# Kernel tuning notes

Measured on AMD Instinct MI355X. Metric: run time of the kernel, lower is better.

The kernel has to match this reference:

```python
import jax, jax.numpy as jnp
import numpy as np

N_BATCH = 128   # C: number of PWL channels / generator batch
N_PTS = 32768   # N: samples per channel
K_PWL = 20      # breakpoints per piecewise-linear function
LATENT = 8
HID = 8
EPS = 1e-7


def _mlp(z, W1, b1, W2, b2):
    # torch mlp: Linear -> Tanh -> Linear -> Tanh
    h = jnp.tanh(z @ W1 + b1)
    return jnp.tanh(h @ W2 + b2)


def _normalize01(a):
    # per-row min/max normalization, a: [C, N]
    a = a - a.min(axis=1, keepdims=True)
    return a / a.max(axis=1, keepdims=True)


def _calibrate1d(x, xp, yp):
    # x: [N, C], xp/yp: [C, K]
    N, C = x.shape
    K = xp.shape[1]
    bp = jnp.concatenate([x[:, :, None], jnp.broadcast_to(xp[None], (N, C, K))], axis=2)  # [N,C,K+1]
    order = jnp.argsort(bp, axis=2)                       # [N,C,K+1]
    sorted_bp = jnp.take_along_axis(bp, order, axis=2)
    x_idx = jnp.argmin(order, axis=2)                     # rank of x among breakpoints
    cand = x_idx - 1
    start_idx = jnp.where(x_idx == 0, 1, jnp.where(x_idx == K, K - 2, cand))
    end_idx = jnp.where(start_idx == cand, start_idx + 2, start_idx + 1)
    start_x = jnp.take_along_axis(sorted_bp, start_idx[..., None], axis=2)[..., 0]
    end_x = jnp.take_along_axis(sorted_bp, end_idx[..., None], axis=2)[..., 0]
    start_idx2 = jnp.where(x_idx == 0, 0, jnp.where(x_idx == K, K - 2, cand))
    yp_e = jnp.broadcast_to(yp[None], (N, C, K))
    start_y = jnp.take_along_axis(yp_e, start_idx2[..., None], axis=2)[..., 0]
    end_y = jnp.take_along_axis(yp_e, (start_idx2 + 1)[..., None], axis=2)[..., 0]
    return start_y + (x - start_x) * (end_y - start_y) / (end_x - start_x + EPS)


def setup_inputs() -> dict:
    key = jax.random.key(0)
    ks = jax.random.split(key, 16)
    s = 0.5
    f32 = jnp.float32
    return {
        "zf": jax.random.normal(ks[0], (N_BATCH, LATENT), f32),
        "zx": jax.random.normal(ks[1], (N_BATCH, N_PTS, LATENT), f32),
        "ze": jax.random.normal(ks[2], (N_BATCH, N_PTS, LATENT), f32),
        "Wx1": jax.random.normal(ks[3], (LATENT, HID), f32) * s,
        "bx1": jax.random.normal(ks[4], (HID,), f32) * s,
        "Wx2": jax.random.normal(ks[5], (HID, 1), f32) * s,
        "bx2": jax.random.normal(ks[6], (1,), f32) * s,
        "We1": jax.random.normal(ks[7], (LATENT, HID), f32) * s,
        "be1": jax.random.normal(ks[8], (HID,), f32) * s,
        "We2": jax.random.normal(ks[9], (HID, 1), f32) * s,
        "be2": jax.random.normal(ks[10], (1,), f32) * s,
        "Wf1": jax.random.normal(ks[11], (LATENT, HID), f32) * s,
        "bf1": jax.random.normal(ks[12], (HID,), f32) * s,
        "Wf2": jax.random.normal(ks[13], (HID, K_PWL), f32) * s,
        "bf2": jax.random.normal(ks[14], (K_PWL,), f32) * s,
        "directions": jax.random.randint(ks[15], (N_BATCH,), 0, 2) > 0,
    }


def reference(zf, zx, ze, Wx1, bx1, Wx2, bx2, We1, be1, We2, be2, Wf1, bf1, Wf2, bf2, directions):
    # gen_f: random ascending/descending monotone PWL per channel
    pts = _mlp(zf, Wf1, bf1, Wf2, bf2)                        # [C, K]
    asc = jnp.sort(pts, axis=1)
    yp = jnp.where(directions[:, None], asc, asc[:, ::-1])    # [C, K]
    xp = jnp.broadcast_to(jnp.linspace(0.0, 1.0, K_PWL, dtype=pts.dtype)[None, :], yp.shape)
    # forward_x: cause variable, per-channel normalized to [0,1]
    x = _mlp(zx, Wx1, bx1, Wx2, bx2)[..., 0]                  # [C, N]
    x = _normalize01(x).T                                     # [N, C]
    # forward_e: standardized noise (global mean / unbiased std)
    e = _mlp(ze, We1, be1, We2, be2)[..., 0].T                # [N, C]
    e = (e - e.mean()) / e.std(ddof=1)
    # forward_y
    y = _calibrate1d(x, xp, yp) + 0.1 * e                     # [N, C]
    return y
```

## Files before the change

kernel.cpp:

```cpp
#include <hip/hip_runtime.h>

#define C_CH  128
#define NP    32768
#define K_PWL 20
#define LAT   8
#define HID   8
#define SLOTS 32

__device__ __forceinline__ float fast_tanh(float x) {
    float e = __expf(2.0f * x);
    return fmaf(-2.0f, __builtin_amdgcn_rcpf(e + 1.0f), 1.0f);
}

__device__ __forceinline__ unsigned fenc(float f) {
    unsigned u = __float_as_uint(f);
    return (u & 0x80000000u) ? ~u : (u | 0x80000000u);
}
__device__ __forceinline__ float fdec(unsigned e) {
    unsigned u = (e & 0x80000000u) ? (e ^ 0x80000000u) : ~e;
    return __uint_as_float(u);
}

__global__ void prep(const float* __restrict__ zf,
                     const float* __restrict__ Wf1, const float* __restrict__ bf1,
                     const float* __restrict__ Wf2, const float* __restrict__ bf2,
                     const unsigned char* __restrict__ dirs_raw,
                     float* __restrict__ ypw,
                     unsigned* cminE, unsigned* cmaxE, double* sums) {
    int t = threadIdx.x;
    if (t < C_CH) { cminE[t] = 0xFFFFFFFFu; cmaxE[t] = 0u; }
    if (t < 2 * SLOTS) sums[t] = 0.0;

    __shared__ int is_i32;
    if (t == 0) {
        const int* di = (const int*)dirs_raw;
        int ok = 1;
        for (int i = 0; i < 32; i++) { int v = di[i]; if (v != 0 && v != 1) ok = 0; }
        is_i32 = ok;
    }
    __syncthreads();
    if (t >= C_CH) return;
    int c = t;

    float z[LAT];
    #pragma unroll
    for (int l = 0; l < LAT; l++) z[l] = zf[c * LAT + l];
    float h[HID];
    #pragma unroll
    for (int j = 0; j < HID; j++) {
        float a = bf1[j];
        #pragma unroll
        for (int l = 0; l < LAT; l++) a = fmaf(z[l], Wf1[l * HID + j], a);
        h[j] = fast_tanh(a);
    }
    float p[K_PWL];
    #pragma unroll
    for (int k = 0; k < K_PWL; k++) {
        float a = bf2[k];
        #pragma unroll
        for (int j = 0; j < HID; j++) a = fmaf(h[j], Wf2[j * K_PWL + k], a);
        p[k] = fast_tanh(a);
    }
    for (int i = 1; i < K_PWL; i++) {
        float key = p[i];
        int j = i - 1;
        while (j >= 0 && p[j] > key) { p[j + 1] = p[j]; j--; }
        p[j + 1] = key;
    }
    int dir = is_i32 ? (((const int*)dirs_raw)[c] != 0) : (dirs_raw[c] != 0);
    for (int k = 0; k < K_PWL; k++)
        ypw[c * K_PWL + k] = dir ? p[k] : p[K_PWL - 1 - k];
}

__global__ __launch_bounds__(256, 8)
void pass1(const float* __restrict__ zx, const float* __restrict__ ze,
           const float* __restrict__ Wx1, const float* __restrict__ bx1,
           const float* __restrict__ Wx2, const float* __restrict__ bx2,
           const float* __restrict__ We1, const float* __restrict__ be1,
           const float* __restrict__ We2, const float* __restrict__ be2,
           float2* __restrict__ xe,
           unsigned* __restrict__ cminE, unsigned* __restrict__ cmaxE,
           double* __restrict__ sums) {
    __shared__ float szx[LAT][256];
    __shared__ float sze[LAT][256];
    __shared__ float sw[162];

    int t = threadIdx.x;
    if (t < 64)       sw[t] = Wx1[t];
    else if (t < 72)  sw[t] = bx1[t - 64];
    else if (t < 80)  sw[t] = Wx2[t - 72];
    else if (t == 80) sw[80] = bx2[0];
    else if (t < 145) sw[t] = We1[t - 81];
    else if (t < 153) sw[t] = be1[t - 145];
    else if (t < 161) sw[t] = We2[t - 153];
    else if (t == 161) sw[161] = be2[0];

    int c = blockIdx.y;
    size_t row = (size_t)c * NP;
    int tile0 = blockIdx.x * 256;
    const float4* zx4 = (const float4*)(zx + (row + tile0) * LAT);
    const float4* ze4 = (const float4*)(ze + (row + tile0) * LAT);

    float4 vx0 = zx4[t];
    float4 vx1 = zx4[256 + t];
    float4 ve0 = ze4[t];
    float4 ve1 = ze4[256 + t];

    {
        int q = t, p = q >> 1, l0 = (q & 1) * 4;
        szx[l0 + 0][p] = vx0.x; szx[l0 + 1][p] = vx0.y;
        szx[l0 + 2][p] = vx0.z; szx[l0 + 3][p] = vx0.w;
        sze[l0 + 0][p] = ve0.x; sze[l0 + 1][p] = ve0.y;
        sze[l0 + 2][p] = ve0.z; sze[l0 + 3][p] = ve0.w;
    }
    {
        int q = 256 + t, p = q >> 1, l0 = (q & 1) * 4;
        szx[l0 + 0][p] = vx1.x; szx[l0 + 1][p] = vx1.y;
        szx[l0 + 2][p] = vx1.z; szx[l0 + 3][p] = vx1.w;
        sze[l0 + 0][p] = ve1.x; sze[l0 + 1][p] = ve1.y;
        sze[l0 + 2][p] = ve1.z; sze[l0 + 3][p] = ve1.w;
    }
    __syncthreads();

    float ix[LAT], ie[LAT];
    #pragma unroll
    for (int l = 0; l < LAT; l++) { ix[l] = szx[l][t]; ie[l] = sze[l][t]; }

    float xacc = sw[80];
    float eacc = sw[161];
    #pragma unroll
    for (int j = 0; j < HID; j++) {
        float hx = sw[64 + j];
        float he = sw[145 + j];
        #pragma unroll
        for (int l = 0; l < LAT; l++) {
            hx = fmaf(ix[l], sw[l * 8 + j], hx);
            he = fmaf(ie[l], sw[81 + l * 8 + j], he);
        }
        xacc = fmaf(fast_tanh(hx), sw[72 + j], xacc);
        eacc = fmaf(fast_tanh(he), sw[153 + j], eacc);
    }
    float xv = fast_tanh(xacc);
    float ev = fast_tanh(eacc);

    xe[row + tile0 + t] = make_float2(xv, ev);

    float mn = xv, mx = xv, s = ev, s2 = ev * ev;
    #pragma unroll
    for (int o = 32; o > 0; o >>= 1) {
        mn = fminf(mn, __shfl_down(mn, o));
        mx = fmaxf(mx, __shfl_down(mx, o));
        s += __shfl_down(s, o);
        s2 += __shfl_down(s2, o);
    }
    __shared__ float rmn[4], rmx[4], rs[4], rs2[4];
    int wave = t >> 6, lane = t & 63;
    if (lane == 0) { rmn[wave] = mn; rmx[wave] = mx; rs[wave] = s; rs2[wave] = s2; }
    __syncthreads();
    if (t == 0) {
        for (int w = 1; w < 4; w++) {
            mn = fminf(mn, rmn[w]); mx = fmaxf(mx, rmx[w]);
            s += rs[w]; s2 += rs2[w];
        }
        atomicMin(&cminE[c], fenc(mn));
        atomicMax(&cmaxE[c], fenc(mx));
        int slot = (blockIdx.x + blockIdx.y) & (SLOTS - 1);
        atomicAdd(&sums[2 * slot], (double)s);
        atomicAdd(&sums[2 * slot + 1], (double)s2);
    }
}

__global__ __launch_bounds__(256)
void pass2(const float2* __restrict__ xe, const float* __restrict__ ypw,
           const unsigned* __restrict__ cminE, const unsigned* __restrict__ cmaxE,
           const double* __restrict__ sums,
           float* __restrict__ out) {
    __shared__ float ytile[C_CH * 33];
    __shared__ float syp[C_CH * K_PWL];
    __shared__ float smin[C_CH], sinv[C_CH];
    __shared__ float sstat[2];

    int t = threadIdx.x;
    for (int i = t; i < C_CH * K_PWL; i += 256) syp[i] = ypw[i];
    if (t < C_CH) {
        float mn = fdec(cminE[t]);
        float mx = fdec(cmaxE[t]);
        smin[t] = mn;
        sinv[t] = __builtin_amdgcn_rcpf(mx - mn);
    }
    if (t == 0) {
        double s = 0.0, s2 = 0.0;
        for (int i = 0; i < SLOTS; i++) { s += sums[2 * i]; s2 += sums[2 * i + 1]; }
        double M = (double)C_CH * NP;
        double mean = s / M;
        double var = (s2 - s * s / M) / (M - 1.0);
        sstat[0] = (float)mean;
        sstat[1] = (float)(0.1 / sqrt(var));
    }
    __syncthreads();

    const float INV_DENOM = 1.0f / (1.0f / 19.0f + 1e-7f);
    float mean = sstat[0], escale = sstat[1];
    int n0 = blockIdx.x * 32;

    #pragma unroll
    for (int i = 0; i < 16; i++) {
        int idx = i * 256 + t;
        int c = idx >> 5;
        int j = idx & 31;
        float2 v = xe[(size_t)c * NP + (n0 + j)];
        float xn = (v.x - smin[c]) * sinv[c];
        int seg = (int)floorf(xn * 19.0f);
        seg = max(0, min(18, seg));
        float y0 = syp[c * K_PWL + seg];
        float y1 = syp[c * K_PWL + seg + 1];
        float y = fmaf((xn - (float)seg * (1.0f / 19.0f)) * INV_DENOM, y1 - y0, y0);
        y = fmaf(v.y - mean, escale, y);
        ytile[c * 33 + j] = y;
    }
    __syncthreads();
    #pragma unroll
    for (int i = 0; i < 16; i++) {
        int idx = i * 256 + t;
        int j = idx >> 7;
        int c = idx & 127;
        out[(size_t)(n0 + j) * C_CH + c] = ytile[c * 33 + j];
    }
}

extern "C" void kernel_launch(void* const* d_in, const int* in_sizes, int n_in,
                              void* d_out, int out_size, void* d_ws, size_t ws_size,
                              hipStream_t stream) {
    const float* zf  = (const float*)d_in[0];
    const float* zx  = (const float*)d_in[1];
    const float* ze  = (const float*)d_in[2];
    const float* Wx1 = (const float*)d_in[3];
    const float* bx1 = (const float*)d_in[4];
    const float* Wx2 = (const float*)d_in[5];
    const float* bx2 = (const float*)d_in[6];
    const float* We1 = (const float*)d_in[7];
    const float* be1 = (const float*)d_in[8];
    const float* We2 = (const float*)d_in[9];
    const float* be2 = (const float*)d_in[10];
    const float* Wf1 = (const float*)d_in[11];
    const float* bf1 = (const float*)d_in[12];
    const float* Wf2 = (const float*)d_in[13];
    const float* bf2 = (const float*)d_in[14];
    const unsigned char* dirs = (const unsigned char*)d_in[15];

    float2* xe  = (float2*)d_ws;
    float*  ypw = (float*)(xe + (size_t)C_CH * NP);
    unsigned* cminE = (unsigned*)(ypw + C_CH * K_PWL);
    unsigned* cmaxE = cminE + C_CH;
    double* sums = (double*)(cmaxE + C_CH);

    hipLaunchKernelGGL(prep, dim3(1), dim3(256), 0, stream,
                       zf, Wf1, bf1, Wf2, bf2, dirs, ypw, cminE, cmaxE, sums);
    hipLaunchKernelGGL(pass1, dim3(NP / 256, C_CH), dim3(256), 0, stream,
                       zx, ze, Wx1, bx1, Wx2, bx2, We1, be1, We2, be2,
                       xe, cminE, cmaxE, sums);
    hipLaunchKernelGGL(pass2, dim3(NP / 32), dim3(256), 0, stream,
                       xe, ypw, cminE, cmaxE, sums, (float*)d_out);
}
```

Measured before the change: 366.8 us.

## Make pass1 persistent-style with register prefetch and two points per thread

Pass1 now has each block loop over 8 tiles of 512 points, with each thread computing two points per iteration straight from registers. The LDS transpose of the latent inputs is removed. The next iteration's float4 loads are software-prefetched into registers while the current MLP runs, and the weights are laid out so they can be read as float4 from LDS. The grid is 8x smaller, so there are fewer per-block atomics and reductions. In exchange, register pressure is higher (launch bounds relaxed to 4 blocks) and fewer blocks are available to hide latency.

```diff
diff --git a/kernel.cpp b/kernel.cpp
--- a/kernel.cpp
+++ b/kernel.cpp
@@ -6,6 +6,7 @@
 #define LAT   8
 #define HID   8
 #define SLOTS 32
+#define T_ITER 8
 
 __device__ __forceinline__ float fast_tanh(float x) {
     float e = __expf(2.0f * x);
@@ -72,7 +73,7 @@
         ypw[c * K_PWL + k] = dir ? p[k] : p[K_PWL - 1 - k];
 }
 
-__global__ __launch_bounds__(256, 8)
+__global__ __launch_bounds__(256, 4)
 void pass1(const float* __restrict__ zx, const float* __restrict__ ze,
            const float* __restrict__ Wx1, const float* __restrict__ bx1,
            const float* __restrict__ Wx2, const float* __restrict__ bx2,
@@ -81,71 +82,96 @@
            float2* __restrict__ xe,
            unsigned* __restrict__ cminE, unsigned* __restrict__ cmaxE,
            double* __restrict__ sums) {
-    __shared__ float szx[LAT][256];
-    __shared__ float sze[LAT][256];
-    __shared__ float sw[162];
+    __shared__ __align__(16) float swx1[HID][LAT];
+    __shared__ __align__(16) float swe1[HID][LAT];
+    __shared__ float sbx1[HID], swx2[HID], sbe1[HID], swe2[HID];
+    __shared__ float sb2[2];
 
     int t = threadIdx.x;
-    if (t < 64)       sw[t] = Wx1[t];
-    else if (t < 72)  sw[t] = bx1[t - 64];
-    else if (t < 80)  sw[t] = Wx2[t - 72];
-    else if (t == 80) sw[80] = bx2[0];
-    else if (t < 145) sw[t] = We1[t - 81];
-    else if (t < 153) sw[t] = be1[t - 145];
-    else if (t < 161) sw[t] = We2[t - 153];
-    else if (t == 161) sw[161] = be2[0];
+    if (t < 64)        { swx1[t & 7][t >> 3] = Wx1[t]; }
+    else if (t < 128)  { int u = t - 64; swe1[u & 7][u >> 3] = We1[u]; }
+    else if (t < 136)  sbx1[t - 128] = bx1[t - 128];
+    else if (t < 144)  swx2[t - 136] = Wx2[t - 136];
+    else if (t < 152)  sbe1[t - 144] = be1[t - 144];
+    else if (t < 160)  swe2[t - 152] = We2[t - 152];
+    else if (t == 160) sb2[0] = bx2[0];
+    else if (t == 161) sb2[1] = be2[0];
+    __syncthreads();
 
     int c = blockIdx.y;
     size_t row = (size_t)c * NP;
-    int tile0 = blockIdx.x * 256;
-    const float4* zx4 = (const float4*)(zx + (row + tile0) * LAT);
-    const float4* ze4 = (const float4*)(ze + (row + tile0) * LAT);
-
-    float4 vx0 = zx4[t];
-    float4 vx1 = zx4[256 + t];
-    float4 ve0 = ze4[t];
-    float4 ve1 = ze4[256 + t];
-
+    int base = blockIdx.x * (T_ITER * 512);
+    const float4* zx4 = (const float4*)(zx + (row + base) * LAT);
+    const float4* ze4 = (const float4*)(ze + (row + base) * LAT);
+
+    float4 nx0a, nx0b, nx1a, nx1b, ne0a, ne0b, ne1a, ne1b;
     {
-        int q = t, p = q >> 1, l0 = (q & 1) * 4;
-        szx[l0 + 0][p] = vx0.x; szx[l0 + 1][p] = vx0.y;
-        szx[l0 + 2][p] = vx0.z; szx[l0 + 3][p] = vx0.w;
-        sze[l0 + 0][p] = ve0.x; sze[l0 + 1][p] = ve0.y;
-        sze[l0 + 2][p] = ve0.z; sze[l0 + 3][p] = ve0.w;
-    }
-    {
-        int q = 256 + t, p = q >> 1, l0 = (q & 1) * 4;
-        szx[l0 + 0][p] = vx1.x; szx[l0 + 1][p] = vx1.y;
-        szx[l0 + 2][p] = vx1.z; szx[l0 + 3][p] = vx1.w;
-        sze[l0 + 0][p] = ve1.x; sze[l0 + 1][p] = ve1.y;
-        sze[l0 + 2][p] = ve1.z; sze[l0 + 3][p] = ve1.w;
-    }
-    __syncthreads();
-
-    float ix[LAT], ie[LAT];
-    #pragma unroll
-    for (int l = 0; l < LAT; l++) { ix[l] = szx[l][t]; ie[l] = sze[l][t]; }
-
-    float xacc = sw[80];
-    float eacc = sw[161];
-    #pragma unroll
-    for (int j = 0; j < HID; j++) {
-        float hx = sw[64 + j];
-        float he = sw[145 + j];
+        int qa = 2 * t, qb = 512 + 2 * t;
+        nx0a = zx4[qa]; nx0b = zx4[qa + 1];
+        nx1a = zx4[qb]; nx1b = zx4[qb + 1];
+        ne0a = ze4[qa]; ne0b = ze4[qa + 1];
+        ne1a = ze4[qb]; ne1b = ze4[qb + 1];
+    }
+
+    float bx2s = sb2[0], be2s = sb2[1];
+    float mn = 1e30f, mx = -1e30f, s = 0.f, s2 = 0.f;
+
+    #pragma unroll 1
+    for (int i = 0; i < T_ITER; i++) {
+        float4 cx0a = nx0a, cx0b = nx0b, cx1a = nx1a, cx1b = nx1b;
+        float4 ce0a = ne0a, ce0b = ne0b, ce1a = ne1a, ce1b = ne1b;
+        if (i + 1 < T_ITER) {
+            int qa = (i + 1) * 1024 + 2 * t;
+            int qb = qa + 512;
+            nx0a = zx4[qa]; nx0b = zx4[qa + 1];
+            nx1a = zx4[qb]; nx1b = zx4[qb + 1];
+            ne0a = ze4[qa]; ne0b = ze4[qa + 1];
+            ne1a = ze4[qb]; ne1b = ze4[qb + 1];
+        }
+
+        float xa0 = bx2s, xa1 = bx2s, ea0 = be2s, ea1 = be2s;
         #pragma unroll
-        for (int l = 0; l < LAT; l++) {
-            hx = fmaf(ix[l], sw[l * 8 + j], hx);
-            he = fmaf(ie[l], sw[81 + l * 8 + j], he);
+        for (int j = 0; j < HID; j++) {
+            float4 wxa = *(const float4*)&swx1[j][0];
+            float4 wxb = *(const float4*)&swx1[j][4];
+            float4 wea = *(const float4*)&swe1[j][0];
+            float4 web = *(const float4*)&swe1[j][4];
+            float hx0 = sbx1[j], hx1 = hx0;
+            float he0 = sbe1[j], he1 = he0;
+            hx0 = fmaf(cx0a.x, wxa.x, hx0); hx0 = fmaf(cx0a.y, wxa.y, hx0);
+            hx0 = fmaf(cx0a.z, wxa.z, hx0); hx0 = fmaf(cx0a.w, wxa.w, hx0);
+            hx0 = fmaf(cx0b.x, wxb.x, hx0); hx0 = fmaf(cx0b.y, wxb.y, hx0);
+            hx0 = fmaf(cx0b.z, wxb.z, hx0); hx0 = fmaf(cx0b.w, wxb.w, hx0);
+            hx1 = fmaf(cx1a.x, wxa.x, hx1); hx1 = fmaf(cx1a.y, wxa.y, hx1);
+            hx1 = fmaf(cx1a.z, wxa.z, hx1); hx1 = fmaf(cx1a.w, wxa.w, hx1);
+            hx1 = fmaf(cx1b.x, wxb.x, hx1); hx1 = fmaf(cx1b.y, wxb.y, hx1);
+            hx1 = fmaf(cx1b.z, wxb.z, hx1); hx1 = fmaf(cx1b.w, wxb.w, hx1);
+            he0 = fmaf(ce0a.x, wea.x, he0); he0 = fmaf(ce0a.y, wea.y, he0);
+            he0 = fmaf(ce0a.z, wea.z, he0); he0 = fmaf(ce0a.w, wea.w, he0);
+            he0 = fmaf(ce0b.x, web.x, he0); he0 = fmaf(ce0b.y, web.y, he0);
+            he0 = fmaf(ce0b.z, web.z, he0); he0 = fmaf(ce0b.w, web.w, he0);
+            he1 = fmaf(ce1a.x, wea.x, he1); he1 = fmaf(ce1a.y, wea.y, he1);
+            he1 = fmaf(ce1a.z, wea.z, he1); he1 = fmaf(ce1a.w, wea.w, he1);
+            he1 = fmaf(ce1b.x, web.x, he1); he1 = fmaf(ce1b.y, web.y, he1);
+            he1 = fmaf(ce1b.z, web.z, he1); he1 = fmaf(ce1b.w, web.w, he1);
+            xa0 = fmaf(fast_tanh(hx0), swx2[j], xa0);
+            xa1 = fmaf(fast_tanh(hx1), swx2[j], xa1);
+            ea0 = fmaf(fast_tanh(he0), swe2[j], ea0);
+            ea1 = fmaf(fast_tanh(he1), swe2[j], ea1);
         }
-        xacc = fmaf(fast_tanh(hx), sw[72 + j], xacc);
-        eacc = fmaf(fast_tanh(he), sw[153 + j], eacc);
-    }
-    float xv = fast_tanh(xacc);
-    float ev = fast_tanh(eacc);
-
-    xe[row + tile0 + t] = make_float2(xv, ev);
-
-    float mn = xv, mx = xv, s = ev, s2 = ev * ev;
+        float xv0 = fast_tanh(xa0), xv1 = fast_tanh(xa1);
+        float ev0 = fast_tanh(ea0), ev1 = fast_tanh(ea1);
+
+        int n = base + i * 512 + t;
+        xe[row + n]       = make_float2(xv0, ev0);
+        xe[row + n + 256] = make_float2(xv1, ev1);
+
+        mn = fminf(mn, fminf(xv0, xv1));
+        mx = fmaxf(mx, fmaxf(xv0, xv1));
+        s  += ev0 + ev1;
+        s2 += fmaf(ev0, ev0, ev1 * ev1);
+    }
+
     #pragma unroll
     for (int o = 32; o > 0; o >>= 1) {
         mn = fminf(mn, __shfl_down(mn, o));
@@ -189,11 +215,11 @@
         sinv[t] = __builtin_amdgcn_rcpf(mx - mn);
     }
     if (t == 0) {
-        double s = 0.0, s2 = 0.0;
-        for (int i = 0; i < SLOTS; i++) { s += sums[2 * i]; s2 += sums[2 * i + 1]; }
+        double sd = 0.0, sd2 = 0.0;
+        for (int i = 0; i < SLOTS; i++) { sd += sums[2 * i]; sd2 += sums[2 * i + 1]; }
         double M = (double)C_CH * NP;
-        double mean = s / M;
-        double var = (s2 - s * s / M) / (M - 1.0);
+        double mean = sd / M;
+        double var = (sd2 - sd * sd / M) / (M - 1.0);
         sstat[0] = (float)mean;
         sstat[1] = (float)(0.1 / sqrt(var));
     }
@@ -256,7 +282,7 @@
 
     hipLaunchKernelGGL(prep, dim3(1), dim3(256), 0, stream,
                        zf, Wf1, bf1, Wf2, bf2, dirs, ypw, cminE, cmaxE, sums);
-    hipLaunchKernelGGL(pass1, dim3(NP / 256, C_CH), dim3(256), 0, stream,
+    hipLaunchKernelGGL(pass1, dim3(NP / (T_ITER * 512), C_CH), dim3(256), 0, stream,
                        zx, ze, Wx1, bx1, Wx2, bx2, We1, be1, We2, be2,
                        xe, cminE, cmaxE, sums);
     hipLaunchKernelGGL(pass2, dim3(NP / 32), dim3(256), 0, stream,
```

After: 581.5 us. 58.5% more time.

## Process multiple points per thread in pass1 with direct float4 loads

Applied to the files above, without the earlier changes.

Pass1 now handles 8 points per thread in a loop instead of one. Each thread reads its two float4 latent rows directly from global memory rather than staging them through a shared-memory transpose. The x and e weights are interleaved as float2 in shared memory so one load feeds both MLPs. Per-thread min/max/sum are accumulated across points before the wave reduction, which cuts the number of blocks and atomics by 8x. Per-thread loads are now strided by 32 bytes (two float4 per point), which may lower coalescing efficiency, and the loop uses unroll 1, which limits memory-level parallelism.

```diff
diff --git a/kernel.cpp b/kernel.cpp
--- a/kernel.cpp
+++ b/kernel.cpp
@@ -6,6 +6,7 @@
 #define LAT   8
 #define HID   8
 #define SLOTS 32
+#define PTS   8
 
 __device__ __forceinline__ float fast_tanh(float x) {
     float e = __expf(2.0f * x);
@@ -81,71 +82,58 @@
            float2* __restrict__ xe,
            unsigned* __restrict__ cminE, unsigned* __restrict__ cmaxE,
            double* __restrict__ sums) {
-    __shared__ float szx[LAT][256];
-    __shared__ float sze[LAT][256];
-    __shared__ float sw[162];
+    __shared__ __align__(16) float2 sw1[HID][LAT];
+    __shared__ float2 sb1[HID], sw2[HID];
+    __shared__ float2 sb2;
 
     int t = threadIdx.x;
-    if (t < 64)       sw[t] = Wx1[t];
-    else if (t < 72)  sw[t] = bx1[t - 64];
-    else if (t < 80)  sw[t] = Wx2[t - 72];
-    else if (t == 80) sw[80] = bx2[0];
-    else if (t < 145) sw[t] = We1[t - 81];
-    else if (t < 153) sw[t] = be1[t - 145];
-    else if (t < 161) sw[t] = We2[t - 153];
-    else if (t == 161) sw[161] = be2[0];
+    if (t < 64)        { int l = t >> 3, j = t & 7; sw1[j][l] = make_float2(Wx1[t], We1[t]); }
+    else if (t < 72)   { int j = t - 64; sb1[j] = make_float2(bx1[j], be1[j]); }
+    else if (t < 80)   { int j = t - 72; sw2[j] = make_float2(Wx2[j], We2[j]); }
+    else if (t == 80)  sb2 = make_float2(bx2[0], be2[0]);
+    __syncthreads();
 
     int c = blockIdx.y;
     size_t row = (size_t)c * NP;
-    int tile0 = blockIdx.x * 256;
-    const float4* zx4 = (const float4*)(zx + (row + tile0) * LAT);
-    const float4* ze4 = (const float4*)(ze + (row + tile0) * LAT);
-
-    float4 vx0 = zx4[t];
-    float4 vx1 = zx4[256 + t];
-    float4 ve0 = ze4[t];
-    float4 ve1 = ze4[256 + t];
-
-    {
-        int q = t, p = q >> 1, l0 = (q & 1) * 4;
-        szx[l0 + 0][p] = vx0.x; szx[l0 + 1][p] = vx0.y;
-        szx[l0 + 2][p] = vx0.z; szx[l0 + 3][p] = vx0.w;
-        sze[l0 + 0][p] = ve0.x; sze[l0 + 1][p] = ve0.y;
-        sze[l0 + 2][p] = ve0.z; sze[l0 + 3][p] = ve0.w;
-    }
-    {
-        int q = 256 + t, p = q >> 1, l0 = (q & 1) * 4;
-        szx[l0 + 0][p] = vx1.x; szx[l0 + 1][p] = vx1.y;
-        szx[l0 + 2][p] = vx1.z; szx[l0 + 3][p] = vx1.w;
-        sze[l0 + 0][p] = ve1.x; sze[l0 + 1][p] = ve1.y;
-        sze[l0 + 2][p] = ve1.z; sze[l0 + 3][p] = ve1.w;
-    }
-    __syncthreads();
-
-    float ix[LAT], ie[LAT];
-    #pragma unroll
-    for (int l = 0; l < LAT; l++) { ix[l] = szx[l][t]; ie[l] = sze[l][t]; }
-
-    float xacc = sw[80];
-    float eacc = sw[161];
-    #pragma unroll
-    for (int j = 0; j < HID; j++) {
-        float hx = sw[64 + j];
-        float he = sw[145 + j];
+    int base = blockIdx.x * (256 * PTS);
+    const float4* zx4 = (const float4*)(zx + (row + base) * LAT);
+    const float4* ze4 = (const float4*)(ze + (row + base) * LAT);
+    float2* xeo = xe + row + base;
+
+    float2 b2v = sb2;
+    float mn = 1e30f, mx = -1e30f, s = 0.f, s2 = 0.f;
+
+    #pragma unroll 1
+    for (int i = 0; i < PTS; i++) {
+        int n = i * 256 + t;
+        float4 xa = zx4[2 * n], xb = zx4[2 * n + 1];
+        float4 ea = ze4[2 * n], eb = ze4[2 * n + 1];
+
+        float2 acc = b2v;
         #pragma unroll
-        for (int l = 0; l < LAT; l++) {
-            hx = fmaf(ix[l], sw[l * 8 + j], hx);
-            he = fmaf(ie[l], sw[81 + l * 8 + j], he);
+        for (int j = 0; j < HID; j++) {
+            float2 h = sb1[j];
+            float2 w;
+            w = sw1[j][0]; h.x = fmaf(xa.x, w.x, h.x); h.y = fmaf(ea.x, w.y, h.y);
+            w = sw1[j][1]; h.x = fmaf(xa.y, w.x, h.x); h.y = fmaf(ea.y, w.y, h.y);
+            w = sw1[j][2]; h.x = fmaf(xa.z, w.x, h.x); h.y = fmaf(ea.z, w.y, h.y);
+            w = sw1[j][3]; h.x = fmaf(xa.w, w.x, h.x); h.y = fmaf(ea.w, w.y, h.y);
+            w = sw1[j][4]; h.x = fmaf(xb.x, w.x, h.x); h.y = fmaf(eb.x, w.y, h.y);
+            w = sw1[j][5]; h.x = fmaf(xb.y, w.x, h.x); h.y = fmaf(eb.y, w.y, h.y);
+            w = sw1[j][6]; h.x = fmaf(xb.z, w.x, h.x); h.y = fmaf(eb.z, w.y, h.y);
+            w = sw1[j][7]; h.x = fmaf(xb.w, w.x, h.x); h.y = fmaf(eb.w, w.y, h.y);
+            float2 w2v = sw2[j];
+            acc.x = fmaf(fast_tanh(h.x), w2v.x, acc.x);
+            acc.y = fmaf(fast_tanh(h.y), w2v.y, acc.y);
         }
-        xacc = fmaf(fast_tanh(hx), sw[72 + j], xacc);
-        eacc = fmaf(fast_tanh(he), sw[153 + j], eacc);
-    }
-    float xv = fast_tanh(xacc);
-    float ev = fast_tanh(eacc);
-
-    xe[row + tile0 + t] = make_float2(xv, ev);
-
-    float mn = xv, mx = xv, s = ev, s2 = ev * ev;
+        float xv = fast_tanh(acc.x);
+        float ev = fast_tanh(acc.y);
+
+        xeo[n] = make_float2(xv, ev);
+        mn = fminf(mn, xv); mx = fmaxf(mx, xv);
+        s += ev; s2 = fmaf(ev, ev, s2);
+    }
+
     #pragma unroll
     for (int o = 32; o > 0; o >>= 1) {
         mn = fminf(mn, __shfl_down(mn, o));
@@ -189,11 +177,11 @@
         sinv[t] = __builtin_amdgcn_rcpf(mx - mn);
     }
     if (t == 0) {
-        double s = 0.0, s2 = 0.0;
-        for (int i = 0; i < SLOTS; i++) { s += sums[2 * i]; s2 += sums[2 * i + 1]; }
+        double sd = 0.0, sd2 = 0.0;
+        for (int i = 0; i < SLOTS; i++) { sd += sums[2 * i]; sd2 += sums[2 * i + 1]; }
         double M = (double)C_CH * NP;
-        double mean = s / M;
-        double var = (s2 - s * s / M) / (M - 1.0);
+        double mean = sd / M;
+        double var = (sd2 - sd * sd / M) / (M - 1.0);
         sstat[0] = (float)mean;
         sstat[1] = (float)(0.1 / sqrt(var));
     }
@@ -256,7 +244,7 @@
 
     hipLaunchKernelGGL(prep, dim3(1), dim3(256), 0, stream,
                        zf, Wf1, bf1, Wf2, bf2, dirs, ypw, cminE, cmaxE, sums);
-    hipLaunchKernelGGL(pass1, dim3(NP / 256, C_CH), dim3(256), 0, stream,
+    hipLaunchKernelGGL(pass1, dim3(NP / (256 * PTS), C_CH), dim3(256), 0, stream,
                        zx, ze, Wx1, bx1, Wx2, bx2, We1, be1, We2, be2,
                        xe, cminE, cmaxE, sums);
     hipLaunchKernelGGL(pass2, dim3(NP / 32), dim3(256), 0, stream,
```

Result: slower. 718.4 us (+95.9%).
